# Performance work log

Measured on AMD Instinct MI355X. Metric: run time of the kernel, lower is better.

The kernel has to match this reference:

```python
import jax, jax.numpy as jnp
import numpy as np
from jax import lax

MU = 255
H = 64            # block_hidden_size
SKIP = 256        # skip_size
NUM_LAYERS = 24
CYCLE = 6
UP_CONV = 4       # upsample_convs=[4]
UP_REPEAT = 75
LF = 80           # local_features_size
B = 2
L = 64            # local feature frames
T = L * UP_CONV * UP_REPEAT  # 19200 signal samples


def setup_inputs() -> dict:
    key = jax.random.key(0)
    ks = jax.random.split(key, 16)
    r = lambda k, shape, sc=0.05: jax.random.normal(k, shape, jnp.float32) * sc
    return {
        "local_features": jax.random.normal(ks[0], (B, L, LF), jnp.float32),
        "gold_signal": jax.random.uniform(ks[1], (B, T), jnp.float32, minval=-1.0, maxval=1.0),
        "embed_w": r(ks[2], (H, 1)),
        "embed_b": r(ks[3], (H,)),
        "up_w": r(ks[4], (LF, LF, UP_CONV)),
        "up_b": r(ks[5], (LF,)),
        "proj_w": r(ks[6], (NUM_LAYERS * 2 * H, LF)),
        "proj_b": r(ks[7], (NUM_LAYERS * 2 * H,)),
        "dil_w": r(ks[8], (NUM_LAYERS, 2 * H, H, 2)),
        "dil_b": r(ks[9], (NUM_LAYERS, 2 * H)),
        "skip_w": r(ks[10], (NUM_LAYERS, SKIP, H)),
        "skip_b": r(ks[11], (NUM_LAYERS, SKIP)),
        "res_w": r(ks[12], (NUM_LAYERS - 1, H, H)),
        "res_b": r(ks[13], (NUM_LAYERS - 1, H)),
        "out1_w": r(ks[14], (MU + 1, SKIP)),
        "out2_w": r(ks[15], (MU + 1, MU + 1)),
    }


def _causal_dilated_conv(x, w, b, dilation):
    # x: [B, C, T]; w: [O, C, 2]; left-pad so output[t] depends on inputs <= t
    xp = jnp.pad(x, ((0, 0), (0, 0), (dilation, 0)))
    y = lax.conv_general_dilated(xp, w, window_strides=(1,), padding="VALID",
                                 rhs_dilation=(dilation,),
                                 dimension_numbers=("NCH", "OIH", "NCH"))
    return y + b[None, :, None]


def _upsample(local_features, up_w, up_b, proj_w, proj_b):
    # local_features: [B, L, LF] -> cond [B, NUM_LAYERS, 2H, T]
    x = jnp.transpose(local_features, (0, 2, 1))  # [B, LF, L]
    # ConvTranspose1d with kernel_size == stride == UP_CONV (no overlap)
    y = jnp.einsum("bfl,fgk->bglk", x, up_w).reshape(x.shape[0], LF, -1)
    y = y + up_b[None, :, None]                                  # [B, LF, L*4]
    # 1x1 projection to per-layer gate conditioning (chunking in the original
    # is a memory trick, math-identical to a single conv)
    z = jnp.einsum("bft,of->bot", y, proj_w) + proj_b[None, :, None]
    z = jnp.repeat(z, UP_REPEAT, axis=-1)                        # [B, NL*2H, T]
    return z.reshape(z.shape[0], NUM_LAYERS, 2 * H, -1)


def reference(local_features, gold_signal, embed_w, embed_b, up_w, up_b,
              proj_w, proj_b, dil_w, dil_b, skip_w, skip_b, res_w, res_b,
              out1_w, out2_w):
    cond = _upsample(local_features, up_w, up_b, proj_w, proj_b)
    # embed: Conv1d(1 -> H, kernel 1)
    x = gold_signal[:, None, :] * embed_w[None, :, :] + embed_b[None, :, None]
    skip_sum = None
    for i in range(NUM_LAYERS):
        dilation = 2 ** (i % CYCLE)
        y = _causal_dilated_conv(x, dil_w[i], dil_b[i], dilation) + cond[:, i]
        gated = jnp.tanh(y[:, :H]) * jax.nn.sigmoid(y[:, H:])
        skip = jnp.einsum("bht,sh->bst", gated, skip_w[i]) + skip_b[i][None, :, None]
        skip_sum = skip if skip_sum is None else skip_sum + skip
        if i < NUM_LAYERS - 1:  # last layer has no residual out_conv
            x = x + jnp.einsum("bht,oh->bot", gated, res_w[i]) + res_b[i][None, :, None]
    h = jnp.einsum("bst,os->bot", jax.nn.relu(skip_sum), out1_w)
    h = jnp.einsum("bst,os->bot", jax.nn.relu(h), out2_w)
    return jax.nn.log_softmax(h, axis=1)  # [B, MU+1, T]
```

## Files before the change

### kernel.cpp

```cpp
#include <hip/hip_runtime.h>
#include <math.h>

#define T_TOT 19200
#define HD    64
#define SKIPN 256
#define NLAYER 24
#define LFN   80
#define NB    2
#define NTL   64
#define HALO  64
#define XR    (NTL + HALO)
#define NGT   (T_TOT / NTL)
#define NOH   32
#define NTH   (T_TOT / NOH)
#define NCH   (T_TOT / 32)

typedef float  f32x4  __attribute__((ext_vector_type(4)));
typedef __bf16 bf16x8 __attribute__((ext_vector_type(8)));
typedef __bf16 bf16x4 __attribute__((ext_vector_type(4)));

__device__ __forceinline__ f32x4 mfma16(bf16x8 a, bf16x8 b, f32x4 c) {
    return __builtin_amdgcn_mfma_f32_16x16x32_bf16(a, b, c, 0, 0, 0);
}

__global__ __launch_bounds__(256) void prep_kernel(
    const float* __restrict__ dil_w, const float* __restrict__ skip_w,
    const float* __restrict__ skip_b, const float* __restrict__ res_w,
    const float* __restrict__ out1_w, const float* __restrict__ out2_w,
    __bf16* __restrict__ A1f, __bf16* __restrict__ Asf, __bf16* __restrict__ A3f,
    __bf16* __restrict__ Ao1f, __bf16* __restrict__ Ao2f, float* __restrict__ sbsum)
{
    int idx = blockIdx.x * 256 + threadIdx.x;
    if (idx < 24 * 128 * 128) {
        {
            int j = idx & 7, lane = (idx >> 3) & 63, ks = (idx >> 9) & 3;
            int mt = (idx >> 11) & 7, l = idx >> 14;
            int row = mt * 16 + (lane & 15);
            int k   = ks * 32 + (lane >> 4) * 8 + j;
            A1f[idx] = (__bf16)dil_w[((l * 128 + row) * 64 + (k & 63)) * 2 + (k >> 6)];
        }
        {
            int j = idx & 7, lane = (idx >> 3) & 63, ks = (idx >> 9) & 1;
            int mt = (idx >> 10) & 15, l = idx >> 14;
            int row = mt * 16 + (lane & 15);
            int k   = ks * 32 + (lane >> 4) * 8 + j;
            Asf[idx] = (__bf16)skip_w[(l * 256 + row) * 64 + k];
        }
    }
    if (idx < 23 * 64 * 64) {
        int j = idx & 7, lane = (idx >> 3) & 63, ks = (idx >> 9) & 1;
        int mt = (idx >> 10) & 3, l = idx >> 12;
        int row = mt * 16 + (lane & 15);
        int k   = ks * 32 + (lane >> 4) * 8 + j;
        A3f[idx] = (__bf16)res_w[(l * 64 + row) * 64 + k];
    }
    if (idx < 256 * 256) {
        int j = idx & 7, lane = (idx >> 3) & 63, ks = (idx >> 9) & 7;
        int mt = idx >> 12;
        int row = mt * 16 + (lane & 15);
        int k   = ks * 32 + (lane >> 4) * 8 + j;
        Ao1f[idx] = (__bf16)out1_w[row * 256 + k];
        Ao2f[idx] = (__bf16)out2_w[row * 256 + k];
    }
    if (idx < 256) {
        float s = 0.0f;
        #pragma unroll
        for (int l = 0; l < NLAYER; ++l) s += skip_b[l * 256 + idx];
        sbsum[idx] = s;
    }
}

__global__ __launch_bounds__(256) void up_kernel(
    const float* __restrict__ lf, const float* __restrict__ up_w,
    const float* __restrict__ up_b, float* __restrict__ y_up)
{
    int idx = blockIdx.x * 256 + threadIdx.x;
    if (idx >= NB * LFN * 256) return;
    int t4 = idx & 255;
    int g  = (idx >> 8) % LFN;
    int b  = idx / (LFN * 256);
    int l = t4 >> 2, k = t4 & 3;
    float acc = up_b[g];
    const float* lfp = lf + (b * 64 + l) * LFN;
    #pragma unroll 8
    for (int f = 0; f < LFN; ++f)
        acc += lfp[f] * up_w[(f * LFN + g) * 4 + k];
    y_up[idx] = acc;
}

__global__ __launch_bounds__(256) void proj_kernel(
    const float* __restrict__ y_up, const float* __restrict__ proj_w,
    const float* __restrict__ proj_b, float* __restrict__ z)
{
    int idx = blockIdx.x * 256 + threadIdx.x;
    if (idx >= NB * 3072 * 256) return;
    int t4 = idx & 255;
    int o  = (idx >> 8) % 3072;
    int b  = idx / (3072 * 256);
    float acc = proj_b[o];
    const float* yp = y_up + b * LFN * 256 + t4;
    const float* wp = proj_w + o * LFN;
    #pragma unroll 8
    for (int g = 0; g < LFN; ++g)
        acc += wp[g] * yp[g * 256];
    z[idx] = acc;
}

__global__ __launch_bounds__(256) void ztrans_kernel(
    const float* __restrict__ z, const float* __restrict__ dil_b,
    float* __restrict__ zt)
{
    __shared__ float tile[32][33];
    const int b  = blockIdx.z;
    const int o0 = blockIdx.x * 32;
    const int q0 = blockIdx.y * 32;
    const int tx = threadIdx.x & 31;
    const int ty = threadIdx.x >> 5;
    #pragma unroll
    for (int k = 0; k < 4; ++k) {
        int o = o0 + ty + k * 8;
        tile[ty + k * 8][tx] = z[((size_t)(b * 3072 + o)) * 256 + q0 + tx];
    }
    __syncthreads();
    #pragma unroll
    for (int k = 0; k < 4; ++k) {
        int q = q0 + ty + k * 8;
        int o = o0 + tx;
        zt[((size_t)(b * 256 + q)) * 3072 + o] = tile[tx][ty + k * 8] + dil_b[o];
    }
}

__global__ __launch_bounds__(256, 3) void layer_group(
    const float* __restrict__ gold, const float* __restrict__ ew,
    const float* __restrict__ eb,
    const __bf16* __restrict__ xg_in, __bf16* __restrict__ xg_out,
    const float* __restrict__ zt, const float* __restrict__ res_b,
    const __bf16* __restrict__ A1f, const __bf16* __restrict__ A3f,
    __bf16* __restrict__ G, int L0, int first, int last)
{
    __shared__ __bf16 xh[XR][72];
    __shared__ __bf16 Gs[XR][72];
    __shared__ float  zs[3][128];

    const int b    = blockIdx.y;
    const int tb   = blockIdx.x;
    const int t0   = tb * NTL;
    const int tid  = threadIdx.x;
    const int lane = tid & 63;
    const int w    = tid >> 6;
    const int n16  = lane & 15;
    const int quad = lane >> 4;
    const int q0   = ((t0 - HALO > 0) ? t0 - HALO : 0) / 75;

    bf16x8 z8;
    #pragma unroll
    for (int u = 0; u < 8; ++u) z8[u] = (__bf16)0.0f;

    if (first) {
        for (int idx = tid; idx < XR * 8; idx += 256) {
            int r = idx >> 3, hc = (idx & 7) * 8;
            int t = t0 - HALO + r;
            bf16x8 v = z8;
            if (t >= 0) {
                float gv = gold[b * T_TOT + t];
                #pragma unroll
                for (int u = 0; u < 8; ++u)
                    v[u] = (__bf16)(gv * ew[hc + u] + eb[hc + u]);
            }
            *(bf16x8*)&xh[r][hc] = v;
        }
    } else {
        for (int idx = tid; idx < XR * 8; idx += 256) {
            int r = idx >> 3, hc = (idx & 7) * 8;
            int t = t0 - HALO + r;
            bf16x8 v = (t >= 0)
                ? *(const bf16x8*)&xg_in[((size_t)b * T_TOT + t) * 64 + hc] : z8;
            *(bf16x8*)&xh[r][hc] = v;
        }
    }

    const bf16x8* A1v = (const bf16x8*)A1f;
    const bf16x8* A3v = (const bf16x8*)A3f;
    f32x4 zero4 = {0.0f, 0.0f, 0.0f, 0.0f};
    const int stj[6] = {0, 0, 0, 1, 2, 4};

    for (int j = 0; j < 6; ++j) {
        const int l = L0 + j;
        const int d = 1 << j;

        for (int idx = tid; idx < 384; idx += 256) {
            int qq = idx >> 7, oo = idx & 127;
            int q = q0 + qq; if (q > 255) q = 255;
            zs[qq][oo] = zt[((size_t)(b * 256 + q)) * 3072 + l * 128 + oo];
        }
        bf16x8 a1a[4], a1b[4];
        #pragma unroll
        for (int ks = 0; ks < 4; ++ks) {
            a1a[ks] = A1v[((l * 8 + w) * 4 + ks) * 64 + lane];
            a1b[ks] = A1v[((l * 8 + 4 + w) * 4 + ks) * 64 + lane];
        }
        __syncthreads();

        for (int nt = stj[j]; nt < 8; ++nt) {
            int nn = nt * 16 + n16;
            int rm = (nn >= d) ? nn - d : 0;
            bf16x8 b0 = *(const bf16x8*)&xh[rm][quad * 8];
            bf16x8 b1 = *(const bf16x8*)&xh[rm][32 + quad * 8];
            bf16x8 b2 = *(const bf16x8*)&xh[nn][quad * 8];
            bf16x8 b3 = *(const bf16x8*)&xh[nn][32 + quad * 8];
            f32x4 aa = zero4, ab = zero4;
            aa = mfma16(a1a[0], b0, aa); ab = mfma16(a1b[0], b0, ab);
            aa = mfma16(a1a[1], b1, aa); ab = mfma16(a1b[1], b1, ab);
            aa = mfma16(a1a[2], b2, aa); ab = mfma16(a1b[2], b2, ab);
            aa = mfma16(a1a[3], b3, aa); ab = mfma16(a1b[3], b3, ab);

            int tt = t0 - HALO + nn;
            int qq = ((tt > 0) ? tt : 0) / 75 - q0;
            int o0 = w * 16 + quad * 4;
            f32x4 za = *(const f32x4*)&zs[qq][o0];
            f32x4 zb = *(const f32x4*)&zs[qq][o0 + 64];
            bf16x4 g4;
            #pragma unroll
            for (int r = 0; r < 4; ++r) {
                float ya = aa[r] + za[r];
                float yb = ab[r] + zb[r];
                float th = 1.0f - 2.0f * __builtin_amdgcn_rcpf(__expf(2.0f * ya) + 1.0f);
                float sg = __builtin_amdgcn_rcpf(1.0f + __expf(-yb));
                g4[r] = (__bf16)(th * sg);
            }
            *(bf16x4*)&Gs[nn][o0] = g4;
        }
        __syncthreads();

        for (int idx = tid; idx < 512; idx += 256) {
            int rr = idx >> 3, hc = (idx & 7) * 8;
            int cb = tb * 2 + (rr >> 5);
            size_t off = ((size_t)(b * NCH + cb) * NLAYER + l) * 2048 + (rr & 31) * 64 + hc;
            *(bf16x8*)&G[off] = *(const bf16x8*)&Gs[HALO + rr][hc];
        }

        if (l < NLAYER - 1) {
            bf16x8 a3[2];
            #pragma unroll
            for (int ks = 0; ks < 2; ++ks)
                a3[ks] = A3v[((l * 4 + w) * 2 + ks) * 64 + lane];
            int o0 = w * 16 + quad * 4;
            f32x4 rb = *(const f32x4*)&res_b[l * 64 + o0];
            for (int nt = stj[j]; nt < 8; ++nt) {
                int nn = nt * 16 + n16;
                bf16x8 g0 = *(const bf16x8*)&Gs[nn][quad * 8];
                bf16x8 g1 = *(const bf16x8*)&Gs[nn][32 + quad * 8];
                f32x4 ar = zero4;
                ar = mfma16(a3[0], g0, ar);
                ar = mfma16(a3[1], g1, ar);
                bf16x4 xo = *(const bf16x4*)&xh[nn][o0];
                bf16x4 xn;
                #pragma unroll
                for (int r = 0; r < 4; ++r)
                    xn[r] = (__bf16)((float)xo[r] + ar[r] + rb[r]);
                *(bf16x4*)&xh[nn][o0] = xn;
            }
        }
    }

    if (!last) {
        __syncthreads();
        for (int idx = tid; idx < 512; idx += 256) {
            int rr = idx >> 3, hc = (idx & 7) * 8;
            *(bf16x8*)&xg_out[((size_t)b * T_TOT + t0 + rr) * 64 + hc] =
                *(const bf16x8*)&xh[HALO + rr][hc];
        }
    }
}

__global__ __launch_bounds__(256, 4) void head_mfma(
    const __bf16* __restrict__ G, const __bf16* __restrict__ Asf,
    const float* __restrict__ sbsum, const __bf16* __restrict__ Ao1f,
    const __bf16* __restrict__ Ao2f, float* __restrict__ out)
{
    __shared__ __bf16 Vs[NOH][264];
    __shared__ float redm[4][2][16];
    __shared__ float reds[4][2][16];

    const int b    = blockIdx.y;
    const int tcb  = blockIdx.x;
    const int t0   = tcb * NOH;
    const int tid  = threadIdx.x;
    const int lane = tid & 63;
    const int w    = tid >> 6;
    const int n16  = lane & 15;
    const int quad = lane >> 4;

    f32x4 zero4 = {0.0f, 0.0f, 0.0f, 0.0f};
    f32x4 acc[4][2];
    #pragma unroll
    for (int mt = 0; mt < 4; ++mt)
        #pragma unroll
        for (int nt = 0; nt < 2; ++nt) acc[mt][nt] = zero4;

    const bf16x8* Asv = (const bf16x8*)Asf;
    const __bf16* Gl  = G + ((size_t)(b * NCH + tcb)) * (NLAYER * 2048);

    bf16x8 gb[4], gn[4];
    #pragma unroll
    for (int p = 0; p < 4; ++p) {
        int ks = p >> 1, nt = p & 1;
        gb[p] = *(const bf16x8*)&Gl[(nt * 16 + n16) * 64 + ks * 32 + quad * 8];
    }
    for (int l = 0; l < NLAYER; ++l) {
        if (l < NLAYER - 1) {
            const __bf16* Gn = Gl + 2048;
            #pragma unroll
            for (int p = 0; p < 4; ++p) {
                int ks = p >> 1, nt = p & 1;
                gn[p] = *(const bf16x8*)&Gn[(nt * 16 + n16) * 64 + ks * 32 + quad * 8];
            }
        }
        #pragma unroll
        for (int ks = 0; ks < 2; ++ks)
            #pragma unroll
            for (int mt = 0; mt < 4; ++mt) {
                bf16x8 af = Asv[((l * 16 + w * 4 + mt) * 2 + ks) * 64 + lane];
                acc[mt][0] = mfma16(af, gb[ks * 2 + 0], acc[mt][0]);
                acc[mt][1] = mfma16(af, gb[ks * 2 + 1], acc[mt][1]);
            }
        #pragma unroll
        for (int p = 0; p < 4; ++p) gb[p] = gn[p];
        Gl += 2048;
    }
    {
        int s0 = w * 64 + quad * 4;
        #pragma unroll
        for (int mt = 0; mt < 4; ++mt)
            #pragma unroll
            for (int nt = 0; nt < 2; ++nt) {
                bf16x4 v4;
                #pragma unroll
                for (int r = 0; r < 4; ++r)
                    v4[r] = (__bf16)fmaxf(acc[mt][nt][r] + sbsum[s0 + mt * 16 + r], 0.0f);
                *(bf16x4*)&Vs[nt * 16 + n16][s0 + mt * 16] = v4;
            }
    }
    __syncthreads();

    const bf16x8* W1v = (const bf16x8*)Ao1f;
    const bf16x8* W2v = (const bf16x8*)Ao2f;

    #pragma unroll
    for (int mt = 0; mt < 4; ++mt)
        #pragma unroll
        for (int nt = 0; nt < 2; ++nt) acc[mt][nt] = zero4;
    #pragma unroll
    for (int ks = 0; ks < 8; ++ks) {
        bf16x8 bfr[2];
        #pragma unroll
        for (int nt = 0; nt < 2; ++nt)
            bfr[nt] = *(const bf16x8*)&Vs[nt * 16 + n16][ks * 32 + quad * 8];
        #pragma unroll
        for (int mt = 0; mt < 4; ++mt) {
            bf16x8 af = W1v[((w * 4 + mt) * 8 + ks) * 64 + lane];
            #pragma unroll
            for (int nt = 0; nt < 2; ++nt)
                acc[mt][nt] = mfma16(af, bfr[nt], acc[mt][nt]);
        }
    }
    __syncthreads();
    #pragma unroll
    for (int mt = 0; mt < 4; ++mt)
        #pragma unroll
        for (int nt = 0; nt < 2; ++nt) {
            int o0 = w * 64 + mt * 16 + quad * 4;
            bf16x4 v4;
            #pragma unroll
            for (int r = 0; r < 4; ++r)
                v4[r] = (__bf16)fmaxf(acc[mt][nt][r], 0.0f);
            *(bf16x4*)&Vs[nt * 16 + n16][o0] = v4;
        }
    __syncthreads();

    #pragma unroll
    for (int mt = 0; mt < 4; ++mt)
        #pragma unroll
        for (int nt = 0; nt < 2; ++nt) acc[mt][nt] = zero4;
    #pragma unroll
    for (int ks = 0; ks < 8; ++ks) {
        bf16x8 bfr[2];
        #pragma unroll
        for (int nt = 0; nt < 2; ++nt)
            bfr[nt] = *(const bf16x8*)&Vs[nt * 16 + n16][ks * 32 + quad * 8];
        #pragma unroll
        for (int mt = 0; mt < 4; ++mt) {
            bf16x8 af = W2v[((w * 4 + mt) * 8 + ks) * 64 + lane];
            #pragma unroll
            for (int nt = 0; nt < 2; ++nt)
                acc[mt][nt] = mfma16(af, bfr[nt], acc[mt][nt]);
        }
    }

    float lmax[2], lsum[2];
    #pragma unroll
    for (int nt = 0; nt < 2; ++nt) {
        float m = -1e30f;
        #pragma unroll
        for (int mt = 0; mt < 4; ++mt)
            #pragma unroll
            for (int r = 0; r < 4; ++r) m = fmaxf(m, acc[mt][nt][r]);
        m = fmaxf(m, __shfl_xor(m, 16, 64));
        m = fmaxf(m, __shfl_xor(m, 32, 64));
        lmax[nt] = m;
    }
    if (quad == 0) {
        #pragma unroll
        for (int nt = 0; nt < 2; ++nt) redm[w][nt][n16] = lmax[nt];
    }
    __syncthreads();
    #pragma unroll
    for (int nt = 0; nt < 2; ++nt) {
        float m = redm[0][nt][n16];
        m = fmaxf(m, redm[1][nt][n16]);
        m = fmaxf(m, redm[2][nt][n16]);
        m = fmaxf(m, redm[3][nt][n16]);
        lmax[nt] = m;
        float s = 0.0f;
        #pragma unroll
        for (int mt = 0; mt < 4; ++mt)
            #pragma unroll
            for (int r = 0; r < 4; ++r) s += __expf(acc[mt][nt][r] - m);
        s += __shfl_xor(s, 16, 64);
        s += __shfl_xor(s, 32, 64);
        lsum[nt] = s;
    }
    if (quad == 0) {
        #pragma unroll
        for (int nt = 0; nt < 2; ++nt) reds[w][nt][n16] = lsum[nt];
    }
    __syncthreads();
    #pragma unroll
    for (int nt = 0; nt < 2; ++nt) {
        float s = reds[0][nt][n16] + reds[1][nt][n16] +
                  reds[2][nt][n16] + reds[3][nt][n16];
        float lse = lmax[nt] + logf(s);
        int t = t0 + nt * 16 + n16;
        #pragma unroll
        for (int mt = 0; mt < 4; ++mt)
            #pragma unroll
            for (int r = 0; r < 4; ++r) {
                int o = w * 64 + mt * 16 + quad * 4 + r;
                out[((size_t)(b * SKIPN + o)) * T_TOT + t] = acc[mt][nt][r] - lse;
            }
    }
}

extern "C" void kernel_launch(void* const* d_in, const int* in_sizes, int n_in,
                              void* d_out, int out_size, void* d_ws, size_t ws_size,
                              hipStream_t stream) {
    const float* lf       = (const float*)d_in[0];
    const float* gold     = (const float*)d_in[1];
    const float* embed_w  = (const float*)d_in[2];
    const float* embed_b  = (const float*)d_in[3];
    const float* up_w     = (const float*)d_in[4];
    const float* up_b     = (const float*)d_in[5];
    const float* proj_w   = (const float*)d_in[6];
    const float* proj_b   = (const float*)d_in[7];
    const float* dil_w    = (const float*)d_in[8];
    const float* dil_b    = (const float*)d_in[9];
    const float* skip_w   = (const float*)d_in[10];
    const float* skip_b   = (const float*)d_in[11];
    const float* res_w    = (const float*)d_in[12];
    const float* res_b    = (const float*)d_in[13];
    const float* out1_w   = (const float*)d_in[14];
    const float* out2_w   = (const float*)d_in[15];

    __bf16* A1f  = (__bf16*)d_ws;
    __bf16* Asf  = A1f + 393216;
    __bf16* A3f  = Asf + 393216;
    __bf16* Ao1f = A3f + 94208;
    __bf16* Ao2f = Ao1f + 65536;
    __bf16* G    = Ao2f + 65536;
    __bf16* xga  = G + (size_t)NB * NCH * NLAYER * 2048;
    __bf16* xgb  = xga + (size_t)NB * T_TOT * HD;
    float*  sbsum = (float*)(xgb + (size_t)NB * T_TOT * HD);
    float*  y_up  = sbsum + 256;
    float*  z     = y_up + NB * LFN * 256;
    float*  zt    = z + NB * 3072 * 256;

    prep_kernel<<<(24 * 128 * 128 + 255) / 256, 256, 0, stream>>>(
        dil_w, skip_w, skip_b, res_w, out1_w, out2_w,
        A1f, Asf, A3f, Ao1f, Ao2f, sbsum);
    up_kernel  <<<(NB * LFN * 256 + 255) / 256, 256, 0, stream>>>(lf, up_w, up_b, y_up);
    proj_kernel<<<(NB * 3072 * 256) / 256,      256, 0, stream>>>(y_up, proj_w, proj_b, z);
    ztrans_kernel<<<dim3(96, 8, NB), 256, 0, stream>>>(z, dil_b, zt);

    const __bf16* xin[4] = { xga, xga, xgb, xga };
    __bf16*       xout[4] = { xga, xgb, xga, xgb };
    for (int g = 0; g < 4; ++g) {
        layer_group<<<dim3(NGT, NB), 256, 0, stream>>>(
            gold, embed_w, embed_b, xin[g], xout[g],
            zt, res_b, A1f, A3f, G,
            6 * g, (g == 0) ? 1 : 0, (g == 3) ? 1 : 0);
    }

    head_mfma<<<dim3(NTH, NB), 256, 0, stream>>>(G, Asf, sbsum, Ao1f, Ao2f, (float*)d_out);
}
```

Baseline: 391.2 us.

## Fuse skip projection into layer groups and store per-group skip partial sums

Moves the skip 1x1 conv (GEMM) from the head kernel into each layer_group kernel, accumulating skip outputs over 6 layers in registers and writing one bf16 partial sum per group. This replaces writing the gated activations for all 24 layers to global memory and reading them back in the head with 4 partial-sum arrays that the head sums, adds bias to and applies ReLU. It adds 64 accumulator registers per thread to layer_group, with the occupancy hint dropped to match. It also adds an extra rounding of the skip partials to bf16 and uses strided, uncoalesced scalar bf16 stores. The z buffer is aliased onto the skipp region, which is only safe because z is consumed before the layer groups write there.

```diff
diff --git a/kernel.cpp b/kernel.cpp
--- a/kernel.cpp
+++ b/kernel.cpp
@@ -13,7 +13,7 @@
 #define NGT   (T_TOT / NTL)
 #define NOH   32
 #define NTH   (T_TOT / NOH)
-#define NCH   (T_TOT / 32)
+#define PSTRIDE ((size_t)NB * SKIPN * T_TOT)
 
 typedef float  f32x4  __attribute__((ext_vector_type(4)));
 typedef __bf16 bf16x8 __attribute__((ext_vector_type(8)));
@@ -130,13 +130,14 @@
     }
 }
 
-__global__ __launch_bounds__(256, 3) void layer_group(
+__global__ __launch_bounds__(256) void layer_group(
     const float* __restrict__ gold, const float* __restrict__ ew,
     const float* __restrict__ eb,
     const __bf16* __restrict__ xg_in, __bf16* __restrict__ xg_out,
     const float* __restrict__ zt, const float* __restrict__ res_b,
     const __bf16* __restrict__ A1f, const __bf16* __restrict__ A3f,
-    __bf16* __restrict__ G, int L0, int first, int last)
+    const __bf16* __restrict__ Asf, __bf16* __restrict__ skipp_g,
+    int L0, int first, int last)
 {
     __shared__ __bf16 xh[XR][72];
     __shared__ __bf16 Gs[XR][72];
@@ -147,7 +148,7 @@
     const int t0   = tb * NTL;
     const int tid  = threadIdx.x;
     const int lane = tid & 63;
-    const int w    = tid >> 6;
+    const int wm   = tid >> 6;
     const int n16  = lane & 15;
     const int quad = lane >> 4;
     const int q0   = ((t0 - HALO > 0) ? t0 - HALO : 0) / 75;
@@ -181,8 +182,15 @@
 
     const bf16x8* A1v = (const bf16x8*)A1f;
     const bf16x8* A3v = (const bf16x8*)A3f;
+    const bf16x8* Asv = (const bf16x8*)Asf;
     f32x4 zero4 = {0.0f, 0.0f, 0.0f, 0.0f};
     const int stj[6] = {0, 0, 0, 1, 2, 4};
+
+    f32x4 sacc[4][4];
+    #pragma unroll
+    for (int mt = 0; mt < 4; ++mt)
+        #pragma unroll
+        for (int sn = 0; sn < 4; ++sn) sacc[mt][sn] = zero4;
 
     for (int j = 0; j < 6; ++j) {
         const int l = L0 + j;
@@ -196,8 +204,8 @@
         bf16x8 a1a[4], a1b[4];
         #pragma unroll
         for (int ks = 0; ks < 4; ++ks) {
-            a1a[ks] = A1v[((l * 8 + w) * 4 + ks) * 64 + lane];
-            a1b[ks] = A1v[((l * 8 + 4 + w) * 4 + ks) * 64 + lane];
+            a1a[ks] = A1v[((l * 8 + wm) * 4 + ks) * 64 + lane];
+            a1b[ks] = A1v[((l * 8 + 4 + wm) * 4 + ks) * 64 + lane];
         }
         __syncthreads();
 
@@ -216,7 +224,7 @@
 
             int tt = t0 - HALO + nn;
             int qq = ((tt > 0) ? tt : 0) / 75 - q0;
-            int o0 = w * 16 + quad * 4;
+            int o0 = wm * 16 + quad * 4;
             f32x4 za = *(const f32x4*)&zs[qq][o0];
             f32x4 zb = *(const f32x4*)&zs[qq][o0 + 64];
             bf16x4 g4;
@@ -232,19 +240,27 @@
         }
         __syncthreads();
 
-        for (int idx = tid; idx < 512; idx += 256) {
-            int rr = idx >> 3, hc = (idx & 7) * 8;
-            int cb = tb * 2 + (rr >> 5);
-            size_t off = ((size_t)(b * NCH + cb) * NLAYER + l) * 2048 + (rr & 31) * 64 + hc;
-            *(bf16x8*)&G[off] = *(const bf16x8*)&Gs[HALO + rr][hc];
+        #pragma unroll
+        for (int ks = 0; ks < 2; ++ks) {
+            bf16x8 bfr[4];
+            #pragma unroll
+            for (int sn = 0; sn < 4; ++sn)
+                bfr[sn] = *(const bf16x8*)&Gs[HALO + sn * 16 + n16][ks * 32 + quad * 8];
+            #pragma unroll
+            for (int mt = 0; mt < 4; ++mt) {
+                bf16x8 af = Asv[((l * 16 + wm * 4 + mt) * 2 + ks) * 64 + lane];
+                #pragma unroll
+                for (int sn = 0; sn < 4; ++sn)
+                    sacc[mt][sn] = mfma16(af, bfr[sn], sacc[mt][sn]);
+            }
         }
 
         if (l < NLAYER - 1) {
             bf16x8 a3[2];
             #pragma unroll
             for (int ks = 0; ks < 2; ++ks)
-                a3[ks] = A3v[((l * 4 + w) * 2 + ks) * 64 + lane];
-            int o0 = w * 16 + quad * 4;
+                a3[ks] = A3v[((l * 4 + wm) * 2 + ks) * 64 + lane];
+            int o0 = wm * 16 + quad * 4;
             f32x4 rb = *(const f32x4*)&res_b[l * 64 + o0];
             for (int nt = stj[j]; nt < 8; ++nt) {
                 int nn = nt * 16 + n16;
@@ -263,6 +279,19 @@
         }
     }
 
+    #pragma unroll
+    for (int mt = 0; mt < 4; ++mt) {
+        int s0 = wm * 64 + mt * 16 + quad * 4;
+        #pragma unroll
+        for (int sn = 0; sn < 4; ++sn) {
+            int t = t0 + sn * 16 + n16;
+            #pragma unroll
+            for (int r = 0; r < 4; ++r)
+                skipp_g[((size_t)(b * SKIPN + s0 + r)) * T_TOT + t] =
+                    (__bf16)sacc[mt][sn][r];
+        }
+    }
+
     if (!last) {
         __syncthreads();
         for (int idx = tid; idx < 512; idx += 256) {
@@ -274,75 +303,33 @@
 }
 
 __global__ __launch_bounds__(256, 4) void head_mfma(
-    const __bf16* __restrict__ G, const __bf16* __restrict__ Asf,
-    const float* __restrict__ sbsum, const __bf16* __restrict__ Ao1f,
-    const __bf16* __restrict__ Ao2f, float* __restrict__ out)
+    const __bf16* __restrict__ skipp, const float* __restrict__ sbsum,
+    const __bf16* __restrict__ Ao1f, const __bf16* __restrict__ Ao2f,
+    float* __restrict__ out)
 {
     __shared__ __bf16 Vs[NOH][264];
     __shared__ float redm[4][2][16];
     __shared__ float reds[4][2][16];
 
     const int b    = blockIdx.y;
-    const int tcb  = blockIdx.x;
-    const int t0   = tcb * NOH;
+    const int t0   = blockIdx.x * NOH;
     const int tid  = threadIdx.x;
     const int lane = tid & 63;
     const int w    = tid >> 6;
     const int n16  = lane & 15;
     const int quad = lane >> 4;
 
+    for (int idx = tid; idx < SKIPN * NOH; idx += 256) {
+        int s = idx >> 5, tl = idx & 31;
+        size_t off = ((size_t)(b * SKIPN + s)) * T_TOT + t0 + tl;
+        float v = sbsum[s] + (float)skipp[off] + (float)skipp[off + PSTRIDE] +
+                  (float)skipp[off + 2 * PSTRIDE] + (float)skipp[off + 3 * PSTRIDE];
+        Vs[tl][s] = (__bf16)fmaxf(v, 0.0f);
+    }
+    __syncthreads();
+
     f32x4 zero4 = {0.0f, 0.0f, 0.0f, 0.0f};
     f32x4 acc[4][2];
-    #pragma unroll
-    for (int mt = 0; mt < 4; ++mt)
-        #pragma unroll
-        for (int nt = 0; nt < 2; ++nt) acc[mt][nt] = zero4;
-
-    const bf16x8* Asv = (const bf16x8*)Asf;
-    const __bf16* Gl  = G + ((size_t)(b * NCH + tcb)) * (NLAYER * 2048);
-
-    bf16x8 gb[4], gn[4];
-    #pragma unroll
-    for (int p = 0; p < 4; ++p) {
-        int ks = p >> 1, nt = p & 1;
-        gb[p] = *(const bf16x8*)&Gl[(nt * 16 + n16) * 64 + ks * 32 + quad * 8];
-    }
-    for (int l = 0; l < NLAYER; ++l) {
-        if (l < NLAYER - 1) {
-            const __bf16* Gn = Gl + 2048;
-            #pragma unroll
-            for (int p = 0; p < 4; ++p) {
-                int ks = p >> 1, nt = p & 1;
-                gn[p] = *(const bf16x8*)&Gn[(nt * 16 + n16) * 64 + ks * 32 + quad * 8];
-            }
-        }
-        #pragma unroll
-        for (int ks = 0; ks < 2; ++ks)
-            #pragma unroll
-            for (int mt = 0; mt < 4; ++mt) {
-                bf16x8 af = Asv[((l * 16 + w * 4 + mt) * 2 + ks) * 64 + lane];
-                acc[mt][0] = mfma16(af, gb[ks * 2 + 0], acc[mt][0]);
-                acc[mt][1] = mfma16(af, gb[ks * 2 + 1], acc[mt][1]);
-            }
-        #pragma unroll
-        for (int p = 0; p < 4; ++p) gb[p] = gn[p];
-        Gl += 2048;
-    }
-    {
-        int s0 = w * 64 + quad * 4;
-        #pragma unroll
-        for (int mt = 0; mt < 4; ++mt)
-            #pragma unroll
-            for (int nt = 0; nt < 2; ++nt) {
-                bf16x4 v4;
-                #pragma unroll
-                for (int r = 0; r < 4; ++r)
-                    v4[r] = (__bf16)fmaxf(acc[mt][nt][r] + sbsum[s0 + mt * 16 + r], 0.0f);
-                *(bf16x4*)&Vs[nt * 16 + n16][s0 + mt * 16] = v4;
-            }
-    }
-    __syncthreads();
-
     const bf16x8* W1v = (const bf16x8*)Ao1f;
     const bf16x8* W2v = (const bf16x8*)Ao2f;
 
@@ -476,13 +463,13 @@
     __bf16* A3f  = Asf + 393216;
     __bf16* Ao1f = A3f + 94208;
     __bf16* Ao2f = Ao1f + 65536;
-    __bf16* G    = Ao2f + 65536;
-    __bf16* xga  = G + (size_t)NB * NCH * NLAYER * 2048;
+    __bf16* xga  = Ao2f + 65536;
     __bf16* xgb  = xga + (size_t)NB * T_TOT * HD;
     float*  sbsum = (float*)(xgb + (size_t)NB * T_TOT * HD);
     float*  y_up  = sbsum + 256;
-    float*  z     = y_up + NB * LFN * 256;
-    float*  zt    = z + NB * 3072 * 256;
+    float*  zt    = y_up + NB * LFN * 256;
+    __bf16* skipp = (__bf16*)(zt + NB * 256 * 3072);
+    float*  z     = (float*)skipp;
 
     prep_kernel<<<(24 * 128 * 128 + 255) / 256, 256, 0, stream>>>(
         dil_w, skip_w, skip_b, res_w, out1_w, out2_w,
@@ -496,9 +483,9 @@
     for (int g = 0; g < 4; ++g) {
         layer_group<<<dim3(NGT, NB), 256, 0, stream>>>(
             gold, embed_w, embed_b, xin[g], xout[g],
-            zt, res_b, A1f, A3f, G,
+            zt, res_b, A1f, A3f, Asf, skipp + (size_t)g * PSTRIDE,
             6 * g, (g == 0) ? 1 : 0, (g == 3) ? 1 : 0);
     }
 
-    head_mfma<<<dim3(NTH, NB), 256, 0, stream>>>(G, Asf, sbsum, Ao1f, Ao2f, (float*)d_out);
-}
+    head_mfma<<<dim3(NTH, NB), 256, 0, stream>>>(skipp, sbsum, Ao1f, Ao2f, (float*)d_out);
+}
```

Result: faster. 360.9 us (-7.8%).
